# Optimization experiments

Measured on AMD Instinct MI355X. Metric: run time of the kernel, lower is better.

Reference implementation:

```python
import jax, jax.numpy as jnp
import numpy as np

B, T, C, H = 8, 2048, 1024, 64

def setup_inputs() -> dict:
    key = jax.random.key(0)
    kx, kk, kq, kv = jax.random.split(key, 4)
    x = jax.random.normal(kx, (B, T, C), dtype=jnp.float32)
    # nn.Linear(n_embed, head_size, bias=False) weights stored as [C, H] (already transposed)
    s = 1.0 / np.sqrt(C)
    Wk = jax.random.normal(kk, (C, H), dtype=jnp.float32) * s
    Wq = jax.random.normal(kq, (C, H), dtype=jnp.float32) * s
    Wv = jax.random.normal(kv, (C, H), dtype=jnp.float32) * s
    return {"x": x, "Wk": Wk, "Wq": Wq, "Wv": Wv}

def reference(x, Wk, Wq, Wv):
    Bq, Tq, Cq = x.shape
    k = jnp.einsum('btc,ch->bth', x, Wk)
    q = jnp.einsum('btc,ch->bth', x, Wq)
    v = jnp.einsum('btc,ch->bth', x, Wv)
    # NOTE: faithful to source, which MULTIPLIES by C**0.5 (not 1/sqrt(head_size))
    wei = jnp.einsum('bth,bsh->bts', q, k) * (Cq ** 0.5)  # [B,T,T]
    causal = jnp.tril(jnp.ones((Tq, Tq), dtype=bool))
    wei = jnp.where(causal, wei, -jnp.inf)
    wei = jax.nn.softmax(wei, axis=-1)
    out = jnp.einsum('bts,bsh->bth', wei, v)  # [B,T,H]
    return out
```

## Files before the change

kernel.cpp:

```cpp
#include <hip/hip_runtime.h>

#define TSEQ 2048
#define CDIM 1024
#define HDIM 64
#define NROW (8 * 2048)

typedef __attribute__((ext_vector_type(8))) short bf16x8;
typedef __attribute__((ext_vector_type(4))) float f32x4;

__device__ __forceinline__ unsigned short f2bf(float f) {
    unsigned int u = __builtin_bit_cast(unsigned int, f);
    u = (u + 0x7FFFu + ((u >> 16) & 1u)) >> 16;
    return (unsigned short)u;
}
__device__ __forceinline__ float bf2f(unsigned short h) {
    unsigned int u = ((unsigned int)h) << 16;
    return __builtin_bit_cast(float, u);
}
__device__ __forceinline__ void split2(float v, unsigned short& h, unsigned short& l) {
    h = f2bf(v);
    l = f2bf(v - bf2f(h));
}
__device__ __forceinline__ f32x4 mfma16(bf16x8 a, bf16x8 b, f32x4 c) {
    return __builtin_amdgcn_mfma_f32_16x16x32_bf16(a, b, c, 0, 0, 0);
}
__device__ __forceinline__ void gload_lds16(const unsigned short* g, unsigned short* l) {
    __builtin_amdgcn_global_load_lds(
        (const __attribute__((address_space(1))) unsigned int*)(g),
        (__attribute__((address_space(3))) unsigned int*)(l), 16, 0, 0);
}
__device__ __forceinline__ void gload_lds16f(const float* g, float* l) {
    __builtin_amdgcn_global_load_lds(
        (const __attribute__((address_space(1))) unsigned int*)(g),
        (__attribute__((address_space(3))) unsigned int*)(l), 16, 0, 0);
}

__global__ __launch_bounds__(256) void w_prep(
    const float* __restrict__ Wk, const float* __restrict__ Wq, const float* __restrict__ Wv,
    unsigned short* __restrict__ wThi, unsigned short* __restrict__ wTlo)
{
    __shared__ float tile[64][65];
    const int mm = blockIdx.x >> 4, kt = blockIdx.x & 15;
    const float* __restrict__ W = (mm == 0) ? Wk : (mm == 1) ? Wq : Wv;
    const int t = threadIdx.x;
    #pragma unroll
    for (int s = 0; s < 4; s++) {
        const int f = t + 256 * s;
        const int r = f >> 4, cq = f & 15;
        const float4 wv = *reinterpret_cast<const float4*>(&W[(long)(kt * 64 + r) * HDIM + 4 * cq]);
        tile[4 * cq + 0][r] = wv.x; tile[4 * cq + 1][r] = wv.y;
        tile[4 * cq + 2][r] = wv.z; tile[4 * cq + 3][r] = wv.w;
    }
    __syncthreads();
    const int n = t >> 2, seg = t & 3;
    unsigned short hi[16], lo[16];
    #pragma unroll
    for (int u = 0; u < 16; u++) split2(tile[n][16 * seg + u], hi[u], lo[u]);
    const long base = (long)(mm * 64 + n) * CDIM + kt * 64 + 16 * seg;
    *reinterpret_cast<uint4*>(&wThi[base + 0]) = *reinterpret_cast<uint4*>(&hi[0]);
    *reinterpret_cast<uint4*>(&wThi[base + 8]) = *reinterpret_cast<uint4*>(&hi[8]);
    *reinterpret_cast<uint4*>(&wTlo[base + 0]) = *reinterpret_cast<uint4*>(&lo[0]);
    *reinterpret_cast<uint4*>(&wTlo[base + 8]) = *reinterpret_cast<uint4*>(&lo[8]);
}

__global__ __launch_bounds__(512, 1) void proj_mfma(
    const float* __restrict__ x,
    const unsigned short* __restrict__ wThi, const unsigned short* __restrict__ wTlo,
    unsigned short* __restrict__ khi, unsigned short* __restrict__ klo,
    unsigned short* __restrict__ qhi, unsigned short* __restrict__ qlo,
    unsigned short* __restrict__ vt)
{
    extern __shared__ __align__(16) unsigned char smem[];
    const int t = threadIdx.x;
    const int lane = t & 63, w = t >> 6;
    const int r15 = lane & 15, g = lane >> 4;
    const int wr = w >> 2, wc = w & 3;
    const int bb8 = blockIdx.x & 7, jj = blockIdx.x >> 3;
    const long rowbase = (long)bb8 * TSEQ + jj * 64;

    const unsigned short* wsp[3];
    #pragma unroll
    for (int q = 0; q < 3; q++) {
        const int s = t + 512 * q;
        const int lo = (s >= 768);
        const int s7 = s - 768 * lo;
        const int row = s7 >> 2, sl = s7 & 3;
        wsp[q] = (lo ? wTlo : wThi) + (long)row * CDIM + ((sl ^ ((row >> 2) & 3)) << 3);
    }
    const int xrow_s = t >> 3, xsl_s = t & 7;
    const float* xsp = x + (rowbase + xrow_s) * CDIM + (((xsl_s ^ (xrow_s & 7))) << 2);

    f32x4 acc[2][3];
    #pragma unroll
    for (int mt = 0; mt < 2; mt++)
        #pragma unroll
        for (int nt = 0; nt < 3; nt++) acc[mt][nt] = (f32x4){0.f, 0.f, 0.f, 0.f};

    auto stage = [&](int sl, int kc) {
        unsigned char* base = smem + sl * 32768;
        #pragma unroll
        for (int q = 0; q < 3; q++)
            gload_lds16(wsp[q] + kc, (unsigned short*)(base + (t + 512 * q) * 16));
        gload_lds16f(xsp + kc, (float*)(base + 24576 + t * 16));
    };

    auto compute = [&](int sl) {
        const unsigned short* wb = (const unsigned short*)(smem + sl * 32768);
        const float* xb = (const float*)(smem + sl * 32768 + 24576);
        bf16x8 ah[2], al[2];
        #pragma unroll
        for (int mt = 0; mt < 2; mt++) {
            const int rx = 32 * wr + 16 * mt + r15;
            const int r7 = rx & 7;
            const f32x4 a0 = *reinterpret_cast<const f32x4*>(xb + rx * 32 + (((2 * g) ^ r7) << 2));
            const f32x4 a1 = *reinterpret_cast<const f32x4*>(xb + rx * 32 + (((2 * g + 1) ^ r7) << 2));
            unsigned short h0,h1,h2,h3,h4,h5,h6,h7, l0,l1,l2,l3,l4,l5,l6,l7;
            split2(a0.x, h0, l0); split2(a0.y, h1, l1); split2(a0.z, h2, l2); split2(a0.w, h3, l3);
            split2(a1.x, h4, l4); split2(a1.y, h5, l5); split2(a1.z, h6, l6); split2(a1.w, h7, l7);
            ah[mt] = (bf16x8){(short)h0,(short)h1,(short)h2,(short)h3,(short)h4,(short)h5,(short)h6,(short)h7};
            al[mt] = (bf16x8){(short)l0,(short)l1,(short)l2,(short)l3,(short)l4,(short)l5,(short)l6,(short)l7};
        }
        #pragma unroll
        for (int nt = 0; nt < 3; nt++) {
            const int rw = (3 * wc + nt) * 16 + r15;
            const int cofs = ((g ^ ((rw >> 2) & 3)) << 3);
            const bf16x8 bh = *reinterpret_cast<const bf16x8*>(wb + rw * 32 + cofs);
            const bf16x8 bl = *reinterpret_cast<const bf16x8*>(wb + 6144 + rw * 32 + cofs);
            #pragma unroll
            for (int mt = 0; mt < 2; mt++) {
                acc[mt][nt] = mfma16(ah[mt], bh, acc[mt][nt]);
                acc[mt][nt] = mfma16(al[mt], bh, acc[mt][nt]);
                acc[mt][nt] = mfma16(ah[mt], bl, acc[mt][nt]);
            }
        }
    };

    stage(0, 0);
    stage(1, 32);

    int sA = 0, sB = 1, sC = 2;
    for (int j = 0; j < 32; ++j) {
        if (j < 31) { asm volatile("s_waitcnt vmcnt(4)" ::: "memory"); }
        else        { asm volatile("s_waitcnt vmcnt(0)" ::: "memory"); }
        __builtin_amdgcn_s_barrier();
        asm volatile("" ::: "memory");
        if (j < 30) stage(sC, (j + 2) * 32);
        compute(sA);
        const int tmp = sA; sA = sB; sB = sC; sC = tmp;
    }

    #pragma unroll
    for (int nt = 0; nt < 3; nt++) {
        const int ntg = 3 * wc + nt;
        const int mat = ntg >> 2;
        const int colin = (ntg & 3) * 16 + r15;
        #pragma unroll
        for (int mt = 0; mt < 2; mt++) {
            const int rl = 32 * wr + 16 * mt + 4 * g;
            if (mat == 0) {
                #pragma unroll
                for (int reg = 0; reg < 4; reg++) {
                    unsigned short h, l;
                    split2(acc[mt][nt][reg], h, l);
                    const long idx = (rowbase + rl + reg) * HDIM + colin;
                    khi[idx] = h; klo[idx] = l;
                }
            } else if (mat == 1) {
                #pragma unroll
                for (int reg = 0; reg < 4; reg++) {
                    unsigned short h, l;
                    split2(acc[mt][nt][reg] * 32.0f, h, l);
                    const long idx = (rowbase + rl + reg) * HDIM + colin;
                    qhi[idx] = h; qlo[idx] = l;
                }
            } else {
                ushort4 pk;
                pk.x = f2bf(acc[mt][nt][0]); pk.y = f2bf(acc[mt][nt][1]);
                pk.z = f2bf(acc[mt][nt][2]); pk.w = f2bf(acc[mt][nt][3]);
                const long idx = ((long)bb8 * 64 + colin) * TSEQ + jj * 64 + rl;
                *reinterpret_cast<ushort4*>(&vt[idx]) = pk;
            }
        }
    }
}

__global__ __launch_bounds__(256, 2) void attn_part(
    const unsigned short* __restrict__ khi, const unsigned short* __restrict__ klo,
    const unsigned short* __restrict__ qhi, const unsigned short* __restrict__ qlo,
    const unsigned short* __restrict__ vt,
    float* __restrict__ po, float* __restrict__ pm, float* __restrict__ pl, int nsplit)
{
    __shared__ __align__(16) unsigned short ldsbuf[2][3 * 4096];
    __shared__ __align__(16) unsigned short p_lds4[4][16 * 72];
    const int t = threadIdx.x, w = t >> 6, lane = t & 63;
    const int r15 = lane & 15, g = lane >> 4;
    const int id = blockIdx.x;
    const int b = id & 7;
    const int u = id >> 3;
    const int t5 = u & 31, p = u >> 5;
    int j = (t5 & 1) ? 31 - (t5 >> 1) : (t5 >> 1);
    if (p & 1) j = 31 - j;
    const int n = j + 1;
    const int s = (p * n) / nsplit, e = ((p + 1) * n) / nsplit;
    const int pidx = (b * 32 + j) * nsplit + p;

    if (s >= e) {
        const int rr = t >> 2, cq = (t & 3) * 16;
        if ((t & 3) == 0) { pm[pidx * 64 + rr] = -3e38f; pl[pidx * 64 + rr] = 0.f; }
        const f32x4 z = (f32x4){0.f, 0.f, 0.f, 0.f};
        float* dst = &po[((long)pidx * 64 + rr) * 64 + cq];
        #pragma unroll
        for (int q = 0; q < 4; q++) *reinterpret_cast<f32x4*>(dst + 4 * q) = z;
        return;
    }

    const int row0 = t >> 3;
    const int ce = (((t & 7) ^ (row0 & 7)) << 3);
    const long bkey = (long)b * TSEQ;
    const long vrow = ((long)b * 64 + row0) * TSEQ;
    unsigned short* const lbT = &ldsbuf[0][0];

    auto stage = [&](int cur, int kb) {
        unsigned short* lb = lbT + cur * (3 * 4096) + t * 8;
        const long kgo  = (bkey + (long)kb * 64 + row0) * HDIM + ce;
        const long kgo2 = kgo + 32 * HDIM;
        const long vgo  = vrow + (long)kb * 64 + ce;
        const long vgo2 = vgo + 32L * TSEQ;
        gload_lds16(khi + kgo,  lb);
        gload_lds16(khi + kgo2, lb + 2048);
        gload_lds16(klo + kgo,  lb + 4096);
        gload_lds16(klo + kgo2, lb + 6144);
        gload_lds16(vt  + vgo,  lb + 8192);
        gload_lds16(vt  + vgo2, lb + 10240);
    };

    const long qrow = bkey + (long)j * 64 + 16 * w + r15;
    bf16x8 Qh[2], Ql[2];
    #pragma unroll
    for (int ks = 0; ks < 2; ks++) {
        Qh[ks] = *reinterpret_cast<const bf16x8*>(&qhi[qrow * HDIM + 32 * ks + 8 * g]);
        Ql[ks] = *reinterpret_cast<const bf16x8*>(&qlo[qrow * HDIM + 32 * ks + 8 * g]);
    }

    f32x4 o[4];
    #pragma unroll
    for (int ht = 0; ht < 4; ht++) o[ht] = (f32x4){0.f, 0.f, 0.f, 0.f};
    float m = -3e38f, lsum = 0.f;
    unsigned short* const pw = &p_lds4[w][0];
    const int sw = (r15 & 7) << 4;
    const int c0 = ((16 * g) ^ sw) >> 1;
    const int c1 = ((16 * g + 64) ^ sw) >> 1;

    stage(0, s);
    __syncthreads();

    for (int kb = s; kb < e; ++kb) {
        const int cur = (kb - s) & 1;
        if (kb + 1 < e) stage(cur ^ 1, kb + 1);
        const unsigned short* Kh = lbT + cur * (3 * 4096);
        const unsigned short* Kl = Kh + 4096;
        const unsigned short* Vb = Kh + 8192;
        const bool diag = (kb == j);

        f32x4 sc[4];
        #pragma unroll
        for (int mt = 0; mt < 4; mt++) {
            const bool valid = !diag || (mt <= w);
            f32x4 sv = valid ? (f32x4){0.f, 0.f, 0.f, 0.f}
                             : (f32x4){-1e30f, -1e30f, -1e30f, -1e30f};
            if (valid) {
                const int rb = (16 * mt + r15) * 64;
                const bf16x8 ah0 = *reinterpret_cast<const bf16x8*>(&Kh[rb + c0]);
                const bf16x8 ah1 = *reinterpret_cast<const bf16x8*>(&Kh[rb + c1]);
                const bf16x8 al0 = *reinterpret_cast<const bf16x8*>(&Kl[rb + c0]);
                const bf16x8 al1 = *reinterpret_cast<const bf16x8*>(&Kl[rb + c1]);
                sv = mfma16(ah0, Qh[0], sv);
                sv = mfma16(ah0, Ql[0], sv);
                sv = mfma16(al0, Qh[0], sv);
                sv = mfma16(ah1, Qh[1], sv);
                sv = mfma16(ah1, Ql[1], sv);
                sv = mfma16(al1, Qh[1], sv);
                if (diag && mt == w) {
                    #pragma unroll
                    for (int reg = 0; reg < 4; reg++)
                        if (4 * g + reg > r15) sv[reg] = -1e30f;
                }
            }
            sc[mt] = sv;
        }

        float bml = -3e38f;
        #pragma unroll
        for (int mt = 0; mt < 4; mt++)
            bml = fmaxf(bml, fmaxf(fmaxf(sc[mt][0], sc[mt][1]), fmaxf(sc[mt][2], sc[mt][3])));
        if (!__all(bml - m <= 8.0f)) {
            float bm = fmaxf(bml, __shfl_xor(bml, 16));
            bm = fmaxf(bm, __shfl_xor(bm, 32));
            const float mnew = fmaxf(m, bm);
            const float corr = __expf(m - mnew);
            lsum *= corr;
            #pragma unroll
            for (int ht = 0; ht < 4; ht++) o[ht] *= corr;
            m = mnew;
        }
        #pragma unroll
        for (int mt = 0; mt < 4; mt++) {
            const float p0 = __expf(sc[mt][0] - m);
            const float p1 = __expf(sc[mt][1] - m);
            const float p2 = __expf(sc[mt][2] - m);
            const float p3 = __expf(sc[mt][3] - m);
            lsum += (p0 + p1) + (p2 + p3);
            ushort4 pk;
            pk.x = f2bf(p0); pk.y = f2bf(p1); pk.z = f2bf(p2); pk.w = f2bf(p3);
            *reinterpret_cast<ushort4*>(&pw[r15 * 72 + 16 * mt + 4 * g]) = pk;
        }
        #pragma unroll
        for (int ks = 0; ks < 2; ks++) {
            const bf16x8 pb = *reinterpret_cast<const bf16x8*>(&pw[r15 * 72 + 32 * ks + 8 * g]);
            const int cc = ks ? c1 : c0;
            #pragma unroll
            for (int ht = 0; ht < 4; ht++) {
                const bf16x8 av = *reinterpret_cast<const bf16x8*>(&Vb[(16 * ht + r15) * 64 + cc]);
                o[ht] = mfma16(av, pb, o[ht]);
            }
        }
        __syncthreads();
    }

    lsum += __shfl_xor(lsum, 16);
    lsum += __shfl_xor(lsum, 32);
    if (g == 0) { pm[pidx * 64 + 16 * w + r15] = m; pl[pidx * 64 + 16 * w + r15] = lsum; }
    #pragma unroll
    for (int ht = 0; ht < 4; ht++)
        *reinterpret_cast<f32x4*>(&po[((long)pidx * 64 + 16 * w + r15) * 64 + 16 * ht + 4 * g]) = o[ht];
}

__global__ __launch_bounds__(256) void attn_comb(
    const float* __restrict__ po, const float* __restrict__ pm, const float* __restrict__ pl,
    float* __restrict__ out, int nsplit)
{
    const int t = threadIdx.x;
    const int b = blockIdx.x & 7, j = blockIdx.x >> 3;
    const int r = t >> 2, cq = (t & 3) * 16;
    const int base = (b * 32 + j) * nsplit;

    float M = -3e38f;
    for (int p = 0; p < nsplit; ++p) M = fmaxf(M, pm[(base + p) * 64 + r]);
    float L = 0.f;
    f32x4 acc[4];
    #pragma unroll
    for (int q = 0; q < 4; q++) acc[q] = (f32x4){0.f, 0.f, 0.f, 0.f};
    for (int p = 0; p < nsplit; ++p) {
        const float wp = __expf(pm[(base + p) * 64 + r] - M);
        L += wp * pl[(base + p) * 64 + r];
        const float* src = &po[((long)(base + p) * 64 + r) * 64 + cq];
        #pragma unroll
        for (int q = 0; q < 4; q++) acc[q] += wp * *reinterpret_cast<const f32x4*>(src + 4 * q);
    }
    const float inv = 1.0f / L;
    float* dst = &out[((long)b * TSEQ + j * 64 + r) * HDIM + cq];
    #pragma unroll
    for (int q = 0; q < 4; q++) *reinterpret_cast<f32x4*>(dst + 4 * q) = acc[q] * inv;
}

extern "C" void kernel_launch(void* const* d_in, const int* in_sizes, int n_in,
                              void* d_out, int out_size, void* d_ws, size_t ws_size,
                              hipStream_t stream) {
    const float* x  = (const float*)d_in[0];
    const float* Wk = (const float*)d_in[1];
    const float* Wq = (const float*)d_in[2];
    const float* Wv = (const float*)d_in[3];
    float* outp = (float*)d_out;

    const size_t SZ = (size_t)NROW * HDIM;
    unsigned short* ws   = (unsigned short*)d_ws;
    unsigned short* khi  = ws;
    unsigned short* klo  = ws + 1 * SZ;
    unsigned short* qhi  = ws + 2 * SZ;
    unsigned short* qlo  = ws + 3 * SZ;
    unsigned short* vt   = ws + 4 * SZ;
    unsigned short* wThi = ws + 5 * SZ;
    unsigned short* wTlo = ws + 5 * SZ + 192 * 1024;

    const size_t base_bytes = (5 * SZ + 2 * 192 * 1024) * sizeof(unsigned short);
    int nsplit = 4;
    while (nsplit > 1 && base_bytes + (size_t)nsplit * 4325376 > ws_size) nsplit >>= 1;

    float* po = (float*)((char*)d_ws + base_bytes);
    float* pm = po + (size_t)256 * 64 * 64 * nsplit;
    float* pl = pm + (size_t)256 * 64 * nsplit;

    w_prep<<<48, 256, 0, stream>>>(Wk, Wq, Wv, wThi, wTlo);
    proj_mfma<<<256, 512, 98304, stream>>>(x, wThi, wTlo, khi, klo, qhi, qlo, vt);
    attn_part<<<dim3(256 * nsplit), 256, 0, stream>>>(khi, klo, qhi, qlo, vt, po, pm, pl, nsplit);
    attn_comb<<<256, 256, 0, stream>>>(po, pm, pl, outp, nsplit);
}
```

Baseline: 74.28 us.

## Stream projection weights straight into registers and keep only x in LDS

The projection kernel no longer stages the hi/lo weight tiles in LDS. Each wave now reads its bf16 weight fragments directly from global memory (served by cache) into double-buffered registers, one k-chunk ahead, and only the fp32 x tile goes through a static 3-slot LDS ring. This cuts LDS from 96KB to 24KB and removes the LDS round trip for the weights, in exchange for more per-wave global traffic. The explicit vmcnt waits inside the loop are gone, so the hazard on the async LDS x loads across threads relies on compiler-inserted waits. The bf16 rounding helper is also swapped for the HIP intrinsic.

```diff
diff --git a/kernel.cpp b/kernel.cpp
--- a/kernel.cpp
+++ b/kernel.cpp
@@ -1,4 +1,5 @@
 #include <hip/hip_runtime.h>
+#include <hip/hip_bf16.h>
 
 #define TSEQ 2048
 #define CDIM 1024
@@ -9,17 +10,16 @@
 typedef __attribute__((ext_vector_type(4))) float f32x4;
 
 __device__ __forceinline__ unsigned short f2bf(float f) {
-    unsigned int u = __builtin_bit_cast(unsigned int, f);
-    u = (u + 0x7FFFu + ((u >> 16) & 1u)) >> 16;
-    return (unsigned short)u;
+    return __builtin_bit_cast(unsigned short, __float2bfloat16(f));
 }
 __device__ __forceinline__ float bf2f(unsigned short h) {
     unsigned int u = ((unsigned int)h) << 16;
     return __builtin_bit_cast(float, u);
 }
 __device__ __forceinline__ void split2(float v, unsigned short& h, unsigned short& l) {
-    h = f2bf(v);
-    l = f2bf(v - bf2f(h));
+    __hip_bfloat16 bh = __float2bfloat16(v);
+    h = __builtin_bit_cast(unsigned short, bh);
+    l = f2bf(v - __bfloat162float(bh));
 }
 __device__ __forceinline__ f32x4 mfma16(bf16x8 a, bf16x8 b, f32x4 c) {
     return __builtin_amdgcn_mfma_f32_16x16x32_bf16(a, b, c, 0, 0, 0);
@@ -70,7 +70,7 @@
     unsigned short* __restrict__ qhi, unsigned short* __restrict__ qlo,
     unsigned short* __restrict__ vt)
 {
-    extern __shared__ __align__(16) unsigned char smem[];
+    __shared__ __align__(16) float xlds[3][64 * 32];
     const int t = threadIdx.x;
     const int lane = t & 63, w = t >> 6;
     const int r15 = lane & 15, g = lane >> 4;
@@ -78,17 +78,14 @@
     const int bb8 = blockIdx.x & 7, jj = blockIdx.x >> 3;
     const long rowbase = (long)bb8 * TSEQ + jj * 64;
 
-    const unsigned short* wsp[3];
-    #pragma unroll
-    for (int q = 0; q < 3; q++) {
-        const int s = t + 512 * q;
-        const int lo = (s >= 768);
-        const int s7 = s - 768 * lo;
-        const int row = s7 >> 2, sl = s7 & 3;
-        wsp[q] = (lo ? wTlo : wThi) + (long)row * CDIM + ((sl ^ ((row >> 2) & 3)) << 3);
-    }
-    const int xrow_s = t >> 3, xsl_s = t & 7;
-    const float* xsp = x + (rowbase + xrow_s) * CDIM + (((xsl_s ^ (xrow_s & 7))) << 2);
+    const int xrow_s = t >> 3, xq_s = t & 7;
+    const float* const xsp = x + (rowbase + xrow_s) * CDIM + ((xq_s ^ (xrow_s & 7)) << 2);
+    float* const xslab = &xlds[0][0];
+
+    long wrow[3];
+    #pragma unroll
+    for (int nt = 0; nt < 3; nt++)
+        wrow[nt] = (long)((3 * wc + nt) * 16 + r15) * CDIM + 8 * g;
 
     f32x4 acc[2][3];
     #pragma unroll
@@ -96,17 +93,18 @@
         #pragma unroll
         for (int nt = 0; nt < 3; nt++) acc[mt][nt] = (f32x4){0.f, 0.f, 0.f, 0.f};
 
-    auto stage = [&](int sl, int kc) {
-        unsigned char* base = smem + sl * 32768;
-        #pragma unroll
-        for (int q = 0; q < 3; q++)
-            gload_lds16(wsp[q] + kc, (unsigned short*)(base + (t + 512 * q) * 16));
-        gload_lds16f(xsp + kc, (float*)(base + 24576 + t * 16));
+    auto stageX = [&](int sl, int kc) {
+        gload_lds16f(xsp + kc, xslab + sl * 2048 + t * 4);
     };
-
-    auto compute = [&](int sl) {
-        const unsigned short* wb = (const unsigned short*)(smem + sl * 32768);
-        const float* xb = (const float*)(smem + sl * 32768 + 24576);
+    auto loadW = [&](bf16x8 (&WH)[3], bf16x8 (&WL)[3], int kc) {
+        #pragma unroll
+        for (int nt = 0; nt < 3; nt++) {
+            WH[nt] = *reinterpret_cast<const bf16x8*>(wThi + wrow[nt] + kc);
+            WL[nt] = *reinterpret_cast<const bf16x8*>(wTlo + wrow[nt] + kc);
+        }
+    };
+    auto compute = [&](int sl, const bf16x8 (&BH)[3], const bf16x8 (&BL)[3]) {
+        const float* xb = xslab + sl * 2048;
         bf16x8 ah[2], al[2];
         #pragma unroll
         for (int mt = 0; mt < 2; mt++) {
@@ -121,32 +119,38 @@
             al[mt] = (bf16x8){(short)l0,(short)l1,(short)l2,(short)l3,(short)l4,(short)l5,(short)l6,(short)l7};
         }
         #pragma unroll
-        for (int nt = 0; nt < 3; nt++) {
-            const int rw = (3 * wc + nt) * 16 + r15;
-            const int cofs = ((g ^ ((rw >> 2) & 3)) << 3);
-            const bf16x8 bh = *reinterpret_cast<const bf16x8*>(wb + rw * 32 + cofs);
-            const bf16x8 bl = *reinterpret_cast<const bf16x8*>(wb + 6144 + rw * 32 + cofs);
+        for (int nt = 0; nt < 3; nt++)
             #pragma unroll
             for (int mt = 0; mt < 2; mt++) {
-                acc[mt][nt] = mfma16(ah[mt], bh, acc[mt][nt]);
-                acc[mt][nt] = mfma16(al[mt], bh, acc[mt][nt]);
-                acc[mt][nt] = mfma16(ah[mt], bl, acc[mt][nt]);
+                acc[mt][nt] = mfma16(ah[mt], BH[nt], acc[mt][nt]);
+                acc[mt][nt] = mfma16(al[mt], BH[nt], acc[mt][nt]);
+                acc[mt][nt] = mfma16(ah[mt], BL[nt], acc[mt][nt]);
             }
-        }
     };
 
-    stage(0, 0);
-    stage(1, 32);
+    stageX(0, 0);
+    stageX(1, 32);
+    bf16x8 WAh[3], WAl[3], WBh[3], WBl[3];
+    loadW(WAh, WAl, 0);
+    asm volatile("s_waitcnt vmcnt(0)" ::: "memory");
+    __builtin_amdgcn_s_barrier();
 
     int sA = 0, sB = 1, sC = 2;
-    for (int j = 0; j < 32; ++j) {
-        if (j < 31) { asm volatile("s_waitcnt vmcnt(4)" ::: "memory"); }
-        else        { asm volatile("s_waitcnt vmcnt(0)" ::: "memory"); }
+    #pragma unroll 1
+    for (int i = 0; i < 16; ++i) {
+        const int j = 2 * i;
+        if (j + 2 < 32) stageX(sC, (j + 2) * 32);
+        asm volatile("" ::: "memory");
+        loadW(WBh, WBl, (j + 1) * 32);
+        compute(sA, WAh, WAl);
         __builtin_amdgcn_s_barrier();
+        int tmp = sA; sA = sB; sB = sC; sC = tmp;
+        if (j + 3 < 32) stageX(sC, (j + 3) * 32);
         asm volatile("" ::: "memory");
-        if (j < 30) stage(sC, (j + 2) * 32);
-        compute(sA);
-        const int tmp = sA; sA = sB; sB = sC; sC = tmp;
+        if (j + 2 < 32) loadW(WAh, WAl, (j + 2) * 32);
+        compute(sA, WBh, WBl);
+        __builtin_amdgcn_s_barrier();
+        tmp = sA; sA = sB; sB = sC; sC = tmp;
     }
 
     #pragma unroll
@@ -391,7 +395,7 @@
     float* pl = pm + (size_t)256 * 64 * nsplit;
 
     w_prep<<<48, 256, 0, stream>>>(Wk, Wq, Wv, wThi, wTlo);
-    proj_mfma<<<256, 512, 98304, stream>>>(x, wThi, wTlo, khi, klo, qhi, qlo, vt);
+    proj_mfma<<<256, 512, 0, stream>>>(x, wThi, wTlo, khi, klo, qhi, qlo, vt);
     attn_part<<<dim3(256 * nsplit), 256, 0, stream>>>(khi, klo, qhi, qlo, vt, po, pm, pl, nsplit);
     attn_comb<<<256, 256, 0, stream>>>(po, pm, pl, outp, nsplit);
 }
```

Result: slower. 98.90 us (+33.1%).

## Halve projection row tile, double-buffer with static LDS, raise occupancy

Applied to the files above, without the earlier changes.

The projection kernel now handles 32 rows per block instead of 64, launching 512 blocks with a 56KB static LDS double buffer in place of the 96KB dynamic triple buffer, and declares launch bounds for multiple blocks per CU. The manual vmcnt-based triple-buffer pipeline becomes a simpler stage-next/compute/syncthreads loop. The LDS swizzle changes, and the bf16 conversion now uses the HIP intrinsic. The aim is more resident waves to hide latency. In exchange, W tiles are reloaded twice as often per output row and each step does less MFMA work between barriers.

```diff
diff --git a/kernel.cpp b/kernel.cpp
--- a/kernel.cpp
+++ b/kernel.cpp
@@ -1,4 +1,5 @@
 #include <hip/hip_runtime.h>
+#include <hip/hip_bf16.h>
 
 #define TSEQ 2048
 #define CDIM 1024
@@ -9,17 +10,16 @@
 typedef __attribute__((ext_vector_type(4))) float f32x4;
 
 __device__ __forceinline__ unsigned short f2bf(float f) {
-    unsigned int u = __builtin_bit_cast(unsigned int, f);
-    u = (u + 0x7FFFu + ((u >> 16) & 1u)) >> 16;
-    return (unsigned short)u;
+    return __builtin_bit_cast(unsigned short, __float2bfloat16(f));
 }
 __device__ __forceinline__ float bf2f(unsigned short h) {
     unsigned int u = ((unsigned int)h) << 16;
     return __builtin_bit_cast(float, u);
 }
 __device__ __forceinline__ void split2(float v, unsigned short& h, unsigned short& l) {
-    h = f2bf(v);
-    l = f2bf(v - bf2f(h));
+    __hip_bfloat16 bh = __float2bfloat16(v);
+    h = __builtin_bit_cast(unsigned short, bh);
+    l = f2bf(v - __bfloat162float(bh));
 }
 __device__ __forceinline__ f32x4 mfma16(bf16x8 a, bf16x8 b, f32x4 c) {
     return __builtin_amdgcn_mfma_f32_16x16x32_bf16(a, b, c, 0, 0, 0);
@@ -63,20 +63,20 @@
     *reinterpret_cast<uint4*>(&wTlo[base + 8]) = *reinterpret_cast<uint4*>(&lo[8]);
 }
 
-__global__ __launch_bounds__(512, 1) void proj_mfma(
+__global__ __launch_bounds__(512, 4) void proj_mfma(
     const float* __restrict__ x,
     const unsigned short* __restrict__ wThi, const unsigned short* __restrict__ wTlo,
     unsigned short* __restrict__ khi, unsigned short* __restrict__ klo,
     unsigned short* __restrict__ qhi, unsigned short* __restrict__ qlo,
     unsigned short* __restrict__ vt)
 {
-    extern __shared__ __align__(16) unsigned char smem[];
+    __shared__ __align__(16) unsigned char smem[2][28672];
     const int t = threadIdx.x;
     const int lane = t & 63, w = t >> 6;
     const int r15 = lane & 15, g = lane >> 4;
     const int wr = w >> 2, wc = w & 3;
     const int bb8 = blockIdx.x & 7, jj = blockIdx.x >> 3;
-    const long rowbase = (long)bb8 * TSEQ + jj * 64;
+    const long rowbase = (long)bb8 * TSEQ + jj * 32;
 
     const unsigned short* wsp[3];
     #pragma unroll
@@ -84,69 +84,60 @@
         const int s = t + 512 * q;
         const int lo = (s >= 768);
         const int s7 = s - 768 * lo;
-        const int row = s7 >> 2, sl = s7 & 3;
-        wsp[q] = (lo ? wTlo : wThi) + (long)row * CDIM + ((sl ^ ((row >> 2) & 3)) << 3);
-    }
-    const int xrow_s = t >> 3, xsl_s = t & 7;
-    const float* xsp = x + (rowbase + xrow_s) * CDIM + (((xsl_s ^ (xrow_s & 7))) << 2);
-
-    f32x4 acc[2][3];
-    #pragma unroll
-    for (int mt = 0; mt < 2; mt++)
-        #pragma unroll
-        for (int nt = 0; nt < 3; nt++) acc[mt][nt] = (f32x4){0.f, 0.f, 0.f, 0.f};
+        const int row = s7 >> 2, pq = s7 & 3;
+        wsp[q] = (lo ? wTlo : wThi) + (long)row * CDIM + ((pq ^ ((row >> 1) & 3)) << 3);
+    }
+    const int xrow_s = (t & 255) >> 3, xpq_s = t & 7;
+    const float* const xsp = x + (rowbase + xrow_s) * CDIM + ((xpq_s ^ (xrow_s & 7)) << 2);
+
+    f32x4 acc[3];
+    #pragma unroll
+    for (int nt = 0; nt < 3; nt++) acc[nt] = (f32x4){0.f, 0.f, 0.f, 0.f};
 
     auto stage = [&](int sl, int kc) {
-        unsigned char* base = smem + sl * 32768;
+        unsigned char* base = &smem[sl][0];
         #pragma unroll
         for (int q = 0; q < 3; q++)
             gload_lds16(wsp[q] + kc, (unsigned short*)(base + (t + 512 * q) * 16));
-        gload_lds16f(xsp + kc, (float*)(base + 24576 + t * 16));
+        if (t < 256)
+            gload_lds16f(xsp + kc, (float*)(base + 24576 + t * 16));
     };
 
     auto compute = [&](int sl) {
-        const unsigned short* wb = (const unsigned short*)(smem + sl * 32768);
-        const float* xb = (const float*)(smem + sl * 32768 + 24576);
-        bf16x8 ah[2], al[2];
-        #pragma unroll
-        for (int mt = 0; mt < 2; mt++) {
-            const int rx = 32 * wr + 16 * mt + r15;
+        const unsigned short* wb = (const unsigned short*)&smem[sl][0];
+        const float* xb = (const float*)&smem[sl][24576];
+        bf16x8 ah, al;
+        {
+            const int rx = 16 * wr + r15;
             const int r7 = rx & 7;
             const f32x4 a0 = *reinterpret_cast<const f32x4*>(xb + rx * 32 + (((2 * g) ^ r7) << 2));
             const f32x4 a1 = *reinterpret_cast<const f32x4*>(xb + rx * 32 + (((2 * g + 1) ^ r7) << 2));
             unsigned short h0,h1,h2,h3,h4,h5,h6,h7, l0,l1,l2,l3,l4,l5,l6,l7;
             split2(a0.x, h0, l0); split2(a0.y, h1, l1); split2(a0.z, h2, l2); split2(a0.w, h3, l3);
             split2(a1.x, h4, l4); split2(a1.y, h5, l5); split2(a1.z, h6, l6); split2(a1.w, h7, l7);
-            ah[mt] = (bf16x8){(short)h0,(short)h1,(short)h2,(short)h3,(short)h4,(short)h5,(short)h6,(short)h7};
-            al[mt] = (bf16x8){(short)l0,(short)l1,(short)l2,(short)l3,(short)l4,(short)l5,(short)l6,(short)l7};
+            ah = (bf16x8){(short)h0,(short)h1,(short)h2,(short)h3,(short)h4,(short)h5,(short)h6,(short)h7};
+            al = (bf16x8){(short)l0,(short)l1,(short)l2,(short)l3,(short)l4,(short)l5,(short)l6,(short)l7};
         }
         #pragma unroll
         for (int nt = 0; nt < 3; nt++) {
             const int rw = (3 * wc + nt) * 16 + r15;
-            const int cofs = ((g ^ ((rw >> 2) & 3)) << 3);
+            const int cofs = ((g ^ ((rw >> 1) & 3)) << 3);
             const bf16x8 bh = *reinterpret_cast<const bf16x8*>(wb + rw * 32 + cofs);
             const bf16x8 bl = *reinterpret_cast<const bf16x8*>(wb + 6144 + rw * 32 + cofs);
-            #pragma unroll
-            for (int mt = 0; mt < 2; mt++) {
-                acc[mt][nt] = mfma16(ah[mt], bh, acc[mt][nt]);
-                acc[mt][nt] = mfma16(al[mt], bh, acc[mt][nt]);
-                acc[mt][nt] = mfma16(ah[mt], bl, acc[mt][nt]);
-            }
+            acc[nt] = mfma16(ah, bh, acc[nt]);
+            acc[nt] = mfma16(al, bh, acc[nt]);
+            acc[nt] = mfma16(ah, bl, acc[nt]);
         }
     };
 
     stage(0, 0);
-    stage(1, 32);
-
-    int sA = 0, sB = 1, sC = 2;
+    __syncthreads();
+
     for (int j = 0; j < 32; ++j) {
-        if (j < 31) { asm volatile("s_waitcnt vmcnt(4)" ::: "memory"); }
-        else        { asm volatile("s_waitcnt vmcnt(0)" ::: "memory"); }
-        __builtin_amdgcn_s_barrier();
-        asm volatile("" ::: "memory");
-        if (j < 30) stage(sC, (j + 2) * 32);
-        compute(sA);
-        const int tmp = sA; sA = sB; sB = sC; sC = tmp;
+        const int buf = j & 1;
+        if (j < 31) stage(buf ^ 1, (j + 1) * 32);
+        compute(buf);
+        __syncthreads();
     }
 
     #pragma unroll
@@ -154,32 +145,29 @@
         const int ntg = 3 * wc + nt;
         const int mat = ntg >> 2;
         const int colin = (ntg & 3) * 16 + r15;
-        #pragma unroll
-        for (int mt = 0; mt < 2; mt++) {
-            const int rl = 32 * wr + 16 * mt + 4 * g;
-            if (mat == 0) {
-                #pragma unroll
-                for (int reg = 0; reg < 4; reg++) {
-                    unsigned short h, l;
-                    split2(acc[mt][nt][reg], h, l);
-                    const long idx = (rowbase + rl + reg) * HDIM + colin;
-                    khi[idx] = h; klo[idx] = l;
-                }
-            } else if (mat == 1) {
-                #pragma unroll
-                for (int reg = 0; reg < 4; reg++) {
-                    unsigned short h, l;
-                    split2(acc[mt][nt][reg] * 32.0f, h, l);
-                    const long idx = (rowbase + rl + reg) * HDIM + colin;
-                    qhi[idx] = h; qlo[idx] = l;
-                }
-            } else {
-                ushort4 pk;
-                pk.x = f2bf(acc[mt][nt][0]); pk.y = f2bf(acc[mt][nt][1]);
-                pk.z = f2bf(acc[mt][nt][2]); pk.w = f2bf(acc[mt][nt][3]);
-                const long idx = ((long)bb8 * 64 + colin) * TSEQ + jj * 64 + rl;
-                *reinterpret_cast<ushort4*>(&vt[idx]) = pk;
+        const int rl = 16 * wr + 4 * g;
+        if (mat == 0) {
+            #pragma unroll
+            for (int reg = 0; reg < 4; reg++) {
+                unsigned short h, l;
+                split2(acc[nt][reg], h, l);
+                const long idx = (rowbase + rl + reg) * HDIM + colin;
+                khi[idx] = h; klo[idx] = l;
             }
+        } else if (mat == 1) {
+            #pragma unroll
+            for (int reg = 0; reg < 4; reg++) {
+                unsigned short h, l;
+                split2(acc[nt][reg] * 32.0f, h, l);
+                const long idx = (rowbase + rl + reg) * HDIM + colin;
+                qhi[idx] = h; qlo[idx] = l;
+            }
+        } else {
+            ushort4 pk;
+            pk.x = f2bf(acc[nt][0]); pk.y = f2bf(acc[nt][1]);
+            pk.z = f2bf(acc[nt][2]); pk.w = f2bf(acc[nt][3]);
+            const long idx = ((long)bb8 * 64 + colin) * TSEQ + jj * 32 + rl;
+            *reinterpret_cast<ushort4*>(&vt[idx]) = pk;
         }
     }
 }
@@ -391,7 +379,7 @@
     float* pl = pm + (size_t)256 * 64 * nsplit;
 
     w_prep<<<48, 256, 0, stream>>>(Wk, Wq, Wv, wThi, wTlo);
-    proj_mfma<<<256, 512, 98304, stream>>>(x, wThi, wTlo, khi, klo, qhi, qlo, vt);
+    proj_mfma<<<512, 512, 0, stream>>>(x, wThi, wTlo, khi, klo, qhi, qlo, vt);
     attn_part<<<dim3(256 * nsplit), 256, 0, stream>>>(khi, klo, qhi, qlo, vt, po, pm, pl, nsplit);
     attn_comb<<<256, 256, 0, stream>>>(po, pm, pl, outp, nsplit);
 }
```

After: 73.19 us. Within noise of the previous version (-1.5%).
